# Kernel tuning notes

Measured on AMD Instinct MI355X. Metric: run time of the kernel, lower is better.

Reference implementation:

```python
import jax, jax.numpy as jnp
import numpy as np

BETA = 0.9
THRESHOLD = 1.0
SLOPE = 10.0


def setup_inputs() -> dict:
    key = jax.random.key(0)
    ks = jax.random.split(key, 5)
    B, T, F, H = 32768, 10, 256, 512
    x = jax.random.normal(ks[0], (B, T, F), dtype=jnp.float32)
    W1 = jax.random.normal(ks[1], (H, F), dtype=jnp.float32) * (1.0 / np.sqrt(F))
    b1 = jax.random.normal(ks[2], (H,), dtype=jnp.float32) * 0.01
    W2 = jax.random.normal(ks[3], (1, H), dtype=jnp.float32) * (1.0 / np.sqrt(H))
    b2 = jax.random.normal(ks[4], (1,), dtype=jnp.float32) * 0.01
    return {"x": x, "W1": W1, "b1": b1, "W2": W2, "b2": b2}


def _surrogate_spike(mem):
    return jax.nn.sigmoid(SLOPE * (mem - THRESHOLD))


def _lif(cur, mem):
    mem = BETA * mem + cur
    spike = _surrogate_spike(mem)
    mem = mem - spike * THRESHOLD
    return spike, mem


def reference(x, W1, b1, W2, b2):
    B, T, F = x.shape
    H = W1.shape[0]
    # Precompute fc1 over all time steps in one big GEMM: [B,T,H]
    cur1_all = jnp.einsum('btf,hf->bth', x, W1) + b1

    mem1_0 = jnp.zeros((B, H), dtype=x.dtype)
    mem2_0 = jnp.zeros((B, 1), dtype=x.dtype)

    def step(carry, cur1_t):
        mem1, mem2 = carry
        spk1, mem1 = _lif(cur1_t, mem1)
        cur2 = spk1 @ W2.T + b2  # [B,1]
        spk2, mem2 = _lif(cur2, mem2)
        return (mem1, mem2), spk2

    # scan over the fixed 10 time steps (hard sequential dependency on mem)
    (_, _), spk2_seq = jax.lax.scan(step, (mem1_0, mem2_0),
                                    jnp.moveaxis(cur1_all, 1, 0))  # [T,B,1]
    spk_mean = jnp.sum(spk2_seq, axis=0) / 10.0
    return jax.nn.sigmoid(spk_mean)
```

## Files before the change

### kernel.cpp

```cpp
#include <hip/hip_runtime.h>
#include <hip/hip_bf16.h>


typedef short short8 __attribute__((ext_vector_type(8)));
typedef float f32x4 __attribute__((ext_vector_type(4)));

__device__ __forceinline__ unsigned short bfbits(float f) {
  union { __hip_bfloat16 h; unsigned short u; } c;
  c.h = __float2bfloat16(f);
  return c.u;
}

__device__ __forceinline__ unsigned int bfpack(float a, float b) {
  return (unsigned int)bfbits(a) | ((unsigned int)bfbits(b) << 16);
}

__device__ __forceinline__ float fast_sigmoid(float z) {
  float e = __expf(-z);
  return __builtin_amdgcn_rcpf(1.0f + e);
}

__device__ __forceinline__ void lif4(f32x4& mv, const f32x4 av, float w2c, float pr[4]) {
#pragma unroll
  for (int e = 0; e < 4; ++e) {
    float m   = fmaf(mv[e], 0.9f, av[e]);
    float spk = fast_sigmoid(fmaf(m, 10.f, -10.f));
    mv[e] = m - spk;
    pr[e] = fmaf(spk, w2c, pr[e]);
  }
}

__global__ void w1_to_bf16(const float* __restrict__ w1, unsigned short* __restrict__ o) {
  int i = blockIdx.x * 256 + threadIdx.x;
  float4 v = reinterpret_cast<const float4*>(w1)[i];
  reinterpret_cast<uint2*>(o)[i] = make_uint2(bfpack(v.x, v.y), bfpack(v.z, v.w));
}

__device__ __forceinline__ short8 cvt_frag(const float* p) {
  const float4 v0 = *reinterpret_cast<const float4*>(p);
  const float4 v1 = *reinterpret_cast<const float4*>(p + 4);
  union { unsigned int u[4]; short8 s; } cv;
  cv.u[0] = bfpack(v0.x, v0.y);
  cv.u[1] = bfpack(v0.z, v0.w);
  cv.u[2] = bfpack(v1.x, v1.y);
  cv.u[3] = bfpack(v1.z, v1.w);
  return cv.s;
}

template <bool USE_WS>
__global__
__attribute__((amdgpu_flat_work_group_size(512, 512)))
void snn_main(const float* __restrict__ x,
              const unsigned short* __restrict__ w1bf,
              const float* __restrict__ w1f,
              const float* __restrict__ b1,
              const float* __restrict__ w2,
              const float* __restrict__ b2,
              float* __restrict__ out)
{
  __shared__ __align__(16) float mem_lds[6][512][4];
  __shared__ __align__(16) unsigned short xt[2][2][32][132];
  __shared__ float cur2_lds[10][32][9];

  const int tid  = threadIdx.x;
  const int lane = tid & 63;
  const int wave = tid >> 6;
  const int l15  = lane & 15;
  const int lq   = lane >> 4;
  const long b0  = (long)blockIdx.x * 32;
  const int h0   = wave * 64;

  float w2l[4], b1l[4];
#pragma unroll
  for (int ct = 0; ct < 4; ++ct) {
    int h = h0 + ct * 16 + l15;
    w2l[ct] = w2[h];
    b1l[ct] = b1[h];
  }

#pragma unroll
  for (int p = 0; p < 6; ++p) {
    f32x4 z = {0.f, 0.f, 0.f, 0.f};
    *reinterpret_cast<f32x4*>(&mem_lds[p][tid][0]) = z;
  }
  f32x4 m6 = {0.f, 0.f, 0.f, 0.f}, m7 = m6;

  const int sr = tid >> 4;
  const int sc = tid & 15;
  const float* xrow = x + (b0 + sr) * 2560;

  const unsigned short* wb = w1bf + (h0 + l15) * 256 + lq * 8;
  const float*          wf = w1f  + (h0 + l15) * 256 + lq * 8;

  uint2 pf[4];
#pragma unroll
  for (int j = 0; j < 4; ++j) {
    const float4 v = *reinterpret_cast<const float4*>(xrow + (sc + j * 16) * 4);
    pf[j] = make_uint2(bfpack(v.x, v.y), bfpack(v.z, v.w));
  }

#pragma unroll 1
  for (int t = 0; t < 10; ++t) {
    const int par = t & 1;
#pragma unroll
    for (int j = 0; j < 4; ++j)
      *reinterpret_cast<uint2*>(
          &xt[par][j >> 1][sr][(sc + (j & 1) * 16) * 4]) = pf[j];
    {
      const int tn = (t < 9) ? t + 1 : 9;
#pragma unroll
      for (int j = 0; j < 4; ++j) {
        const float4 v = *reinterpret_cast<const float4*>(
            xrow + tn * 256 + (sc + j * 16) * 4);
        pf[j] = make_uint2(bfpack(v.x, v.y), bfpack(v.z, v.w));
      }
    }
    short8 bfr0[4];
#pragma unroll
    for (int c = 0; c < 4; ++c) {
      if constexpr (USE_WS) bfr0[c] = *reinterpret_cast<const short8*>(wb + c * 4096);
      else                  bfr0[c] = cvt_frag(wf + c * 4096);
    }
    __syncthreads();

    f32x4 acc[2][4];
#pragma unroll
    for (int rt = 0; rt < 2; ++rt)
#pragma unroll
      for (int c = 0; c < 4; ++c) {
        f32x4 cc = { b1l[c], b1l[c], b1l[c], b1l[c] };
        acc[rt][c] = cc;
      }

    __builtin_amdgcn_s_setprio(1);
#pragma unroll
    for (int kk = 0; kk < 8; ++kk) {
      short8 a[2], bfr[4];
#pragma unroll
      for (int rt = 0; rt < 2; ++rt)
        a[rt] = *reinterpret_cast<const short8*>(
            &xt[par][kk >> 2][rt * 16 + l15][(kk & 3) * 32 + lq * 8]);
      if (kk == 0) {
#pragma unroll
        for (int c = 0; c < 4; ++c) bfr[c] = bfr0[c];
      } else {
#pragma unroll
        for (int c = 0; c < 4; ++c) {
          if constexpr (USE_WS)
            bfr[c] = *reinterpret_cast<const short8*>(wb + c * 4096 + kk * 32);
          else
            bfr[c] = cvt_frag(wf + c * 4096 + kk * 32);
        }
      }
#pragma unroll
      for (int rt = 0; rt < 2; ++rt)
#pragma unroll
        for (int c = 0; c < 4; ++c)
          acc[rt][c] = __builtin_amdgcn_mfma_f32_16x16x32_bf16(a[rt], bfr[c], acc[rt][c], 0, 0, 0);
    }
    __builtin_amdgcn_s_setprio(0);

#pragma unroll
    for (int rt = 0; rt < 2; ++rt) {
      float pr[4] = {0.f, 0.f, 0.f, 0.f};
#pragma unroll
      for (int c = 0; c < 4; ++c) {
        const int p = rt * 4 + c;
        if (p < 6) {
          f32x4* slot = reinterpret_cast<f32x4*>(&mem_lds[p][tid][0]);
          f32x4 mv = *slot;
          lif4(mv, acc[rt][c], w2l[c], pr);
          *slot = mv;
        } else if (p == 6) {
          lif4(m6, acc[rt][c], w2l[c], pr);
        } else {
          lif4(m7, acc[rt][c], w2l[c], pr);
        }
      }
#pragma unroll
      for (int e = 0; e < 4; ++e) {
        float v = pr[e];
        v += __shfl_xor(v, 1); v += __shfl_xor(v, 2);
        v += __shfl_xor(v, 4); v += __shfl_xor(v, 8);
        if (l15 == 0) cur2_lds[t][rt * 16 + lq * 4 + e][wave] = v;
      }
    }
  }

  __syncthreads();

  if (tid < 32) {
    const float bias2 = b2[0];
    float mem2 = 0.f, spksum = 0.f;
#pragma unroll
    for (int t = 0; t < 10; ++t) {
      float c2 = bias2;
#pragma unroll
      for (int w = 0; w < 8; ++w) c2 += cur2_lds[t][tid][w];
      float m   = fmaf(mem2, 0.9f, c2);
      float spk = fast_sigmoid(fmaf(m, 10.f, -10.f));
      mem2   = m - spk;
      spksum += spk;
    }
    out[b0 + tid] = fast_sigmoid(spksum * 0.1f);
  }
}

extern "C" void kernel_launch(void* const* d_in, const int* in_sizes, int n_in,
                              void* d_out, int out_size, void* d_ws, size_t ws_size,
                              hipStream_t stream) {
  const float* x  = (const float*)d_in[0];
  const float* W1 = (const float*)d_in[1];
  const float* b1 = (const float*)d_in[2];
  const float* W2 = (const float*)d_in[3];
  const float* b2 = (const float*)d_in[4];
  float* out = (float*)d_out;
  (void)in_sizes; (void)n_in;

  const int grid = out_size / 32;

  if (ws_size >= 512 * 256 * sizeof(unsigned short)) {
    unsigned short* w1bf = (unsigned short*)d_ws;
    w1_to_bf16<<<128, 256, 0, stream>>>(W1, w1bf);
    snn_main<true><<<grid, 512, 0, stream>>>(x, w1bf, W1, b1, W2, b2, out);
  } else {
    snn_main<false><<<grid, 512, 0, stream>>>(x, nullptr, W1, b1, W2, b2, out);
  }
}
```

Measured before the change: 176.9 us.

## Stage first quarter of W1 K-range in LDS and keep one more membrane tile in registers

Copies the first 64 K-columns of bf16 W1 for all 512 hidden units into shared memory once per block. The first two k-steps then read B fragments from LDS instead of global/L2 each time step, and the register-prefetched fragment moves to k-step 2. LDS freed by shrinking mem_lds from 6 to 5 slots lets a third membrane tile live in registers. This trades more LDS and register use, plus a one-time staging load, for less repeated global traffic for W1, with some risk to occupancy.

```diff
diff --git a/kernel.cpp b/kernel.cpp
--- a/kernel.cpp
+++ b/kernel.cpp
@@ -58,8 +58,9 @@
               const float* __restrict__ b2,
               float* __restrict__ out)
 {
-  __shared__ __align__(16) float mem_lds[6][512][4];
+  __shared__ __align__(16) float mem_lds[5][512][4];
   __shared__ __align__(16) unsigned short xt[2][2][32][132];
+  __shared__ __align__(16) unsigned short w1s[512][72];
   __shared__ float cur2_lds[10][32][9];
 
   const int tid  = threadIdx.x;
@@ -79,11 +80,26 @@
   }
 
 #pragma unroll
-  for (int p = 0; p < 6; ++p) {
+  for (int p = 0; p < 5; ++p) {
     f32x4 z = {0.f, 0.f, 0.f, 0.f};
     *reinterpret_cast<f32x4*>(&mem_lds[p][tid][0]) = z;
   }
-  f32x4 m6 = {0.f, 0.f, 0.f, 0.f}, m7 = m6;
+  f32x4 m5 = {0.f, 0.f, 0.f, 0.f}, m6 = m5, m7 = m5;
+
+  if constexpr (USE_WS) {
+    const unsigned short* src = w1bf + tid * 256;
+#pragma unroll
+    for (int j = 0; j < 8; ++j)
+      *reinterpret_cast<uint4*>(&w1s[tid][j * 8]) =
+          *reinterpret_cast<const uint4*>(src + j * 8);
+  } else {
+    const float* src = w1f + tid * 256;
+#pragma unroll
+    for (int j = 0; j < 8; ++j) {
+      short8 s = cvt_frag(src + j * 8);
+      *reinterpret_cast<short8*>(&w1s[tid][j * 8]) = s;
+    }
+  }
 
   const int sr = tid >> 4;
   const int sc = tid & 15;
@@ -118,8 +134,8 @@
     short8 bfr0[4];
 #pragma unroll
     for (int c = 0; c < 4; ++c) {
-      if constexpr (USE_WS) bfr0[c] = *reinterpret_cast<const short8*>(wb + c * 4096);
-      else                  bfr0[c] = cvt_frag(wf + c * 4096);
+      if constexpr (USE_WS) bfr0[c] = *reinterpret_cast<const short8*>(wb + c * 4096 + 2 * 32);
+      else                  bfr0[c] = cvt_frag(wf + c * 4096 + 2 * 32);
     }
     __syncthreads();
 
@@ -140,7 +156,12 @@
       for (int rt = 0; rt < 2; ++rt)
         a[rt] = *reinterpret_cast<const short8*>(
             &xt[par][kk >> 2][rt * 16 + l15][(kk & 3) * 32 + lq * 8]);
-      if (kk == 0) {
+      if (kk < 2) {
+#pragma unroll
+        for (int c = 0; c < 4; ++c)
+          bfr[c] = *reinterpret_cast<const short8*>(
+              &w1s[h0 + c * 16 + l15][kk * 32 + lq * 8]);
+      } else if (kk == 2) {
 #pragma unroll
         for (int c = 0; c < 4; ++c) bfr[c] = bfr0[c];
       } else {
@@ -166,11 +187,13 @@
 #pragma unroll
       for (int c = 0; c < 4; ++c) {
         const int p = rt * 4 + c;
-        if (p < 6) {
+        if (p < 5) {
           f32x4* slot = reinterpret_cast<f32x4*>(&mem_lds[p][tid][0]);
           f32x4 mv = *slot;
           lif4(mv, acc[rt][c], w2l[c], pr);
           *slot = mv;
+        } else if (p == 5) {
+          lif4(m5, acc[rt][c], w2l[c], pr);
         } else if (p == 6) {
           lif4(m6, acc[rt][c], w2l[c], pr);
         } else {
```

New measurement: 174.8 us. About the same (-1.2%).
